# Performance work log

Hardware: AMD Instinct MI355X
Metric: run time of the kernel (lower is better)

Reference implementation:

```python
import jax, jax.numpy as jnp
import numpy as np

VOCAB = 1_000_000
EMBED_DIM = 128
BATCH = 16_384
NOISE_COUNT = 16


def setup_inputs() -> dict:
    key = jax.random.key(0)
    k1, k2, k3, k4, k5, k6 = jax.random.split(key, 6)
    embed = jax.random.uniform(k1, (EMBED_DIM, VOCAB), jnp.float32, -1.0, 1.0)
    bias = jax.random.uniform(k2, (VOCAB, 1), jnp.float32, -1.0, 1.0)
    u = jax.random.uniform(k3, (VOCAB,), jnp.float32, 1e-3, 1.0)
    freq = u / u.sum()  # normalized unigram^0.75 noise distribution
    targets = jax.random.randint(k4, (BATCH,), 0, VOCAB)
    contexts = jax.random.randint(k5, (BATCH,), 0, VOCAB)
    noises = jax.random.randint(k6, (BATCH * NOISE_COUNT,), 0, VOCAB)
    return {"embed": embed, "bias": bias, "freq": freq,
            "targets": targets, "contexts": contexts, "noises": noises,
            "noise_count": NOISE_COUNT}


def reference(embed, bias, freq, targets, contexts, noises, noise_count):
    # embed: (E, V); bias: (V, 1); freq: (V,)
    E = embed.shape[0]
    B = targets.shape[0]
    re = 10.0
    q = embed[:, targets]                      # (E, B) target embeddings
    r = embed[:, contexts]                     # (E, B) context embeddings
    b = bias[targets, 0][None, :]              # (1, B)
    s = ((r * q).sum(0)[None, :] + b) / E      # (1, B) scaled score
    # positive term: log(sigmoid(s - log(k * p(target))))
    pos = jax.nn.log_sigmoid(s - jnp.log(noise_count * freq[targets]))
    loss = pos.sum()
    # noise term: log(1 - sigmoid(tile(s,k) - log(k * p(noise)))) = log_sigmoid(-x)
    s_tiled = jnp.tile(s, (1, noise_count))    # (1, B*k) == torch.cat((s,)*k, dim=1)
    noise_loss = jax.nn.log_sigmoid(-(s_tiled - jnp.log(noise_count * freq[noises]))).sum()
    total_loss = -(loss + noise_loss) / B
    penalty = re * ((q * q).sum() + (r * r).sum()) / (E * B)
    return total_loss + penalty
```

## Files before the change

kernel.cpp:

```cpp
#include <hip/hip_runtime.h>
#include <math.h>


#define PAIRS 32
#define GSPLIT 8

__device__ __forceinline__ float log_sigmoid_f(float x) {
    return fminf(x, 0.0f) - log1pf(expf(-fabsf(x)));
}

__global__ __launch_bounds__(256) void nce_kernel(
    const float* __restrict__ embed,
    const float* __restrict__ bias,
    const float* __restrict__ freq,
    const int*   __restrict__ targets,
    const int*   __restrict__ contexts,
    const int*   __restrict__ noises,
    float*       __restrict__ block_partials,
    int V, int E, int B, int NC)
{
    __shared__ float sh_dot[GSPLIT][PAIRS];
    __shared__ float sh_sq [GSPLIT][PAIRS];
    __shared__ float sh_s  [PAIRS];
    __shared__ float sh_pp [PAIRS];
    __shared__ float sh_n  [GSPLIT][PAIRS];

    const int p = threadIdx.x & (PAIRS - 1);
    const int g = threadIdx.x >> 5;
    const int j = blockIdx.x * PAIRS + p;
    const bool valid = (j < B);

    float dot = 0.0f, sq = 0.0f;
    if (valid) {
        const int t = targets[j];
        const int c = contexts[j];
        const int epc = E / GSPLIT;
        const int e0  = g * epc;
        const float* ct = embed + t;
        const float* cc = embed + c;
        #pragma unroll 8
        for (int e = e0; e < e0 + epc; ++e) {
            float qe = ct[(size_t)e * V];
            float re = cc[(size_t)e * V];
            dot = fmaf(qe, re, dot);
            sq  = fmaf(qe, qe, fmaf(re, re, sq));
        }
    }
    sh_dot[g][p] = dot;
    sh_sq [g][p] = sq;
    __syncthreads();

    if (threadIdx.x < PAIRS) {
        const int jp = blockIdx.x * PAIRS + threadIdx.x;
        float d = 0.0f, s2 = 0.0f;
        #pragma unroll
        for (int gg = 0; gg < GSPLIT; ++gg) {
            d  += sh_dot[gg][threadIdx.x];
            s2 += sh_sq [gg][threadIdx.x];
        }
        float sval = 0.0f, pp = 0.0f;
        if (jp < B) {
            const int t = targets[jp];
            sval = (d + bias[t]) / (float)E;
            const float pos = log_sigmoid_f(sval - logf((float)NC * freq[t]));
            pp = -pos / (float)B + 10.0f * s2 / ((float)E * (float)B);
        }
        sh_s [threadIdx.x] = sval;
        sh_pp[threadIdx.x] = pp;
    }
    __syncthreads();

    float nacc = 0.0f;
    if (valid) {
        const float sval = sh_s[p];
        for (int k = g; k < NC; k += GSPLIT) {
            const int n = noises[j + (size_t)k * B];
            nacc += log_sigmoid_f(-(sval - logf((float)NC * freq[n])));
        }
    }
    sh_n[g][p] = nacc;
    __syncthreads();

    if (threadIdx.x < PAIRS) {
        float a = sh_pp[threadIdx.x];
        float nsum = 0.0f;
        #pragma unroll
        for (int gg = 0; gg < GSPLIT; ++gg) nsum += sh_n[gg][threadIdx.x];
        a += -nsum / (float)B;
        #pragma unroll
        for (int off = 16; off > 0; off >>= 1) a += __shfl_xor(a, off, 64);
        if (threadIdx.x == 0) block_partials[blockIdx.x] = a;
    }
}

__global__ __launch_bounds__(256) void reduce_partials_kernel(
    const float* __restrict__ parts, int n, float* __restrict__ out)
{
    __shared__ double sh[256];
    double a = 0.0;
    for (int i = threadIdx.x; i < n; i += 256) a += (double)parts[i];
    sh[threadIdx.x] = a;
    __syncthreads();
    for (int s = 128; s > 0; s >>= 1) {
        if (threadIdx.x < s) sh[threadIdx.x] += sh[threadIdx.x + s];
        __syncthreads();
    }
    if (threadIdx.x == 0) out[0] = (float)sh[0];
}

extern "C" void kernel_launch(void* const* d_in, const int* in_sizes, int n_in,
                              void* d_out, int out_size, void* d_ws, size_t ws_size,
                              hipStream_t stream) {
    const float* embed    = (const float*)d_in[0];
    const float* bias     = (const float*)d_in[1];
    const float* freq     = (const float*)d_in[2];
    const int*   targets  = (const int*)d_in[3];
    const int*   contexts = (const int*)d_in[4];
    const int*   noises   = (const int*)d_in[5];

    const int V  = in_sizes[2];
    const int E  = in_sizes[0] / V;
    const int B  = in_sizes[3];
    const int NC = in_sizes[5] / B;

    float* partials = (float*)d_ws;

    const int nblocks = (B + PAIRS - 1) / PAIRS;

    nce_kernel<<<nblocks, 256, 0, stream>>>(
        embed, bias, freq, targets, contexts, noises, partials, V, E, B, NC);

    reduce_partials_kernel<<<1, 256, 0, stream>>>(
        partials, nblocks, (float*)d_out);
}
```

Measured before the change: 90.98 us.

## Prefetch noise freq lookups before dot loop and use 16x16 pair split

```diff
diff --git a/kernel.cpp b/kernel.cpp
--- a/kernel.cpp
+++ b/kernel.cpp
@@ -2,8 +2,8 @@
 #include <math.h>
 
 
-#define PAIRS 32
-#define GSPLIT 8
+#define PAIRS 16
+#define GSPLIT 16
 
 __device__ __forceinline__ float log_sigmoid_f(float x) {
     return fminf(x, 0.0f) - log1pf(expf(-fabsf(x)));
@@ -19,21 +19,34 @@
     float*       __restrict__ block_partials,
     int V, int E, int B, int NC)
 {
-    __shared__ float sh_dot[GSPLIT][PAIRS];
-    __shared__ float sh_sq [GSPLIT][PAIRS];
+    __shared__ float sh_dot[PAIRS][GSPLIT + 1];
+    __shared__ float sh_sq [PAIRS][GSPLIT + 1];
     __shared__ float sh_s  [PAIRS];
-    __shared__ float sh_pp [PAIRS];
-    __shared__ float sh_n  [GSPLIT][PAIRS];
+    __shared__ float sh_wred[4];
 
     const int p = threadIdx.x & (PAIRS - 1);
-    const int g = threadIdx.x >> 5;
+    const int g = threadIdx.x >> 4;
     const int j = blockIdx.x * PAIRS + p;
     const bool valid = (j < B);
 
+    float contrib = 0.0f;
+
     float dot = 0.0f, sq = 0.0f;
+    float lg0 = 0.0f;
+    bool  has0 = false;
+    float bval = 0.0f, lgt = 0.0f;
     if (valid) {
         const int t = targets[j];
         const int c = contexts[j];
+        if (g < NC) {
+            const int n = noises[j + (size_t)g * B];
+            lg0 = logf((float)NC * freq[n]);
+            has0 = true;
+        }
+        if (g == 0) {
+            bval = bias[t];
+            lgt  = logf((float)NC * freq[t]);
+        }
         const int epc = E / GSPLIT;
         const int e0  = g * epc;
         const float* ct = embed + t;
@@ -46,51 +59,48 @@
             sq  = fmaf(qe, qe, fmaf(re, re, sq));
         }
     }
-    sh_dot[g][p] = dot;
-    sh_sq [g][p] = sq;
+    sh_dot[p][g] = dot;
+    sh_sq [p][g] = sq;
     __syncthreads();
 
     if (threadIdx.x < PAIRS) {
-        const int jp = blockIdx.x * PAIRS + threadIdx.x;
         float d = 0.0f, s2 = 0.0f;
         #pragma unroll
         for (int gg = 0; gg < GSPLIT; ++gg) {
-            d  += sh_dot[gg][threadIdx.x];
-            s2 += sh_sq [gg][threadIdx.x];
+            d  += sh_dot[threadIdx.x][gg];
+            s2 += sh_sq [threadIdx.x][gg];
         }
-        float sval = 0.0f, pp = 0.0f;
-        if (jp < B) {
-            const int t = targets[jp];
-            sval = (d + bias[t]) / (float)E;
-            const float pos = log_sigmoid_f(sval - logf((float)NC * freq[t]));
-            pp = -pos / (float)B + 10.0f * s2 / ((float)E * (float)B);
+        float sval = 0.0f;
+        if (valid) {
+            sval = (d + bval) / (float)E;
+            const float pos = log_sigmoid_f(sval - lgt);
+            contrib += -pos / (float)B + 10.0f * s2 / ((float)E * (float)B);
         }
-        sh_s [threadIdx.x] = sval;
-        sh_pp[threadIdx.x] = pp;
+        sh_s[threadIdx.x] = sval;
     }
     __syncthreads();
 
-    float nacc = 0.0f;
     if (valid) {
         const float sval = sh_s[p];
-        for (int k = g; k < NC; k += GSPLIT) {
+        float nacc = 0.0f;
+        if (has0) nacc = log_sigmoid_f(-(sval - lg0));
+        for (int k = g + GSPLIT; k < NC; k += GSPLIT) {
             const int n = noises[j + (size_t)k * B];
             nacc += log_sigmoid_f(-(sval - logf((float)NC * freq[n])));
         }
+        contrib += -nacc / (float)B;
     }
-    sh_n[g][p] = nacc;
+
+    #pragma unroll
+    for (int off = 32; off > 0; off >>= 1)
+        contrib += __shfl_xor(contrib, off, 64);
+    const int wave = threadIdx.x >> 6;
+    const int lane = threadIdx.x & 63;
+    if (lane == 0) sh_wred[wave] = contrib;
     __syncthreads();
-
-    if (threadIdx.x < PAIRS) {
-        float a = sh_pp[threadIdx.x];
-        float nsum = 0.0f;
-        #pragma unroll
-        for (int gg = 0; gg < GSPLIT; ++gg) nsum += sh_n[gg][threadIdx.x];
-        a += -nsum / (float)B;
-        #pragma unroll
-        for (int off = 16; off > 0; off >>= 1) a += __shfl_xor(a, off, 64);
-        if (threadIdx.x == 0) block_partials[blockIdx.x] = a;
-    }
+    if (threadIdx.x == 0)
+        block_partials[blockIdx.x] =
+            sh_wred[0] + sh_wred[1] + sh_wred[2] + sh_wred[3];
 }
 
 __global__ __launch_bounds__(256) void reduce_partials_kernel(
```

After: 92.27 us. Within noise of the previous version (+1.4%).
